# Optimization experiments

Measured on AMD Instinct MI355X. Metric: run time of the kernel, lower is better.

The kernel has to match this reference:

```python
import jax, jax.numpy as jnp
import numpy as np
from jax import lax

NPOINT = 1024
NSAMPLE = 32
RADIUS = 0.2
EPS = 1e-5  # BatchNorm eps (torch default)


def farthest_point_sample(xyz, npoint):
    # xyz: [B, N, 3] -> [B, npoint] int32 indices. Deterministic start at index 0
    # (torch version uses a random start; math is otherwise identical).
    B, N, _ = xyz.shape

    def step(carry, _):
        distance, farthest = carry
        centroid = jnp.take_along_axis(xyz, farthest[:, None, None], axis=1)  # [B,1,3]
        d = jnp.sum((xyz - centroid) ** 2, axis=-1)                            # [B,N]
        distance = jnp.minimum(distance, d)
        return (distance, jnp.argmax(distance, axis=-1).astype(jnp.int32)), farthest

    init = (jnp.full((B, N), 1e10, xyz.dtype), jnp.zeros((B,), jnp.int32))
    _, cents = lax.scan(step, init, None, length=npoint)  # [npoint, B]
    return cents.T


def query_ball_point(radius, nsample, xyz, new_xyz):
    # xyz: [B,N,3], new_xyz: [B,S,3] -> [B,S,nsample] int32 indices
    B, N, _ = xyz.shape
    S = new_xyz.shape[1]
    sqr = jnp.sum((new_xyz[:, :, None, :] - xyz[:, None, :, :]) ** 2, axis=-1)  # [B,S,N]
    base = jnp.broadcast_to(jnp.arange(N, dtype=jnp.int32), (B, S, N))
    idx = jnp.where(sqr > radius * radius, N, base)
    idx = jnp.sort(idx, axis=-1)[:, :, :nsample]
    first = idx[:, :, :1]
    return jnp.where(idx == N, first, idx)


def index_points(points, idx):
    # points: [B,N,C], idx: [B,...] -> [B,...,C]
    return jax.vmap(lambda p, i: p[i])(points, idx)


def conv_bn_relu(x, w, b, g, beta):
    # 1x1 Conv2d == per-point linear; BatchNorm2d in training mode (batch stats,
    # biased variance) over all dims except channel.
    y = jnp.einsum('bskc,oc->bsko', x, w) + b          # [B,S,K,O]
    m = jnp.mean(y, axis=(0, 1, 2), keepdims=True)
    v = jnp.var(y, axis=(0, 1, 2), keepdims=True)
    return jax.nn.relu((y - m) / jnp.sqrt(v + EPS) * g + beta)


def setup_inputs() -> dict:
    key = jax.random.key(0)
    ks = jax.random.split(key, 8)
    B, N, D = 16, 4096, 64
    xyz = jax.random.uniform(ks[0], (B, N, 3), dtype=jnp.float32)
    points = jax.random.normal(ks[1], (B, N, D), dtype=jnp.float32)
    chans = [D + 3, 64, 64, 128]
    inp = {'xyz': xyz, 'points': points}
    for i in range(3):
        cin, cout = chans[i], chans[i + 1]
        inp[f'w{i}'] = jax.random.normal(ks[2 + i], (cout, cin), dtype=jnp.float32) * (1.0 / np.sqrt(cin))
        inp[f'b{i}'] = jnp.zeros((cout,), jnp.float32)
        inp[f'g{i}'] = jnp.ones((cout,), jnp.float32)
        inp[f'be{i}'] = jnp.zeros((cout,), jnp.float32)
    return inp


def reference(xyz, points, w0, b0, g0, be0, w1, b1, g1, be1, w2, b2, g2, be2):
    fps_idx = farthest_point_sample(xyz, NPOINT)            # [B,S]
    new_xyz = index_points(xyz, fps_idx)                    # [B,S,3]
    group_idx = query_ball_point(RADIUS, NSAMPLE, xyz, new_xyz)  # [B,S,K]
    grouped_xyz = index_points(xyz, group_idx) - new_xyz[:, :, None, :]  # [B,S,K,3]
    feats = jnp.concatenate([grouped_xyz, index_points(points, group_idx)], axis=-1)
    for (w, b, g, be) in ((w0, b0, g0, be0), (w1, b1, g1, be1), (w2, b2, g2, be2)):
        feats = conv_bn_relu(feats, w, b, g, be)
    new_points = jnp.max(feats, axis=2)                     # max over nsample -> [B,S,C_out]
    return new_xyz, new_points
```

## Files before the change

kernel.cpp:

```cpp
#include <hip/hip_runtime.h>
#include <hip/hip_bf16.h>
#include <cstdint>
#include <cstddef>

#define NPTS   4096
#define NPT    1024
#define NSAMP  32
#define NBATCH 16
#define MROWS  (NBATCH*NPT*NSAMP)
#define EPSV   1e-5f

typedef __attribute__((ext_vector_type(8))) short bfrag;
typedef __attribute__((ext_vector_type(4))) float f32x4;

static __device__ __forceinline__ unsigned short f2bf(float f) {
  union { float f; unsigned u; } x; x.f = f;
  unsigned u = x.u;
  u += 0x7FFFu + ((u >> 16) & 1u);
  return (unsigned short)(u >> 16);
}
static __device__ __forceinline__ float bf2f(unsigned short h) {
  union { unsigned u; float f; } x; x.u = ((unsigned)h) << 16;
  return x.f;
}
static __device__ __forceinline__ unsigned cvt_pk_bf16(float lo, float hi) {
  unsigned r;
  asm("v_cvt_pk_bf16_f32 %0, %1, %2" : "=v"(r) : "v"(lo), "v"(hi));
  return r;
}

__global__ __launch_bounds__(256) void prep_kernel(
    const float* __restrict__ w0, const float* __restrict__ w1,
    const float* __restrict__ w2, unsigned short* __restrict__ wb0,
    unsigned short* __restrict__ wb1, unsigned short* __restrict__ wb2) {
  const int tid = threadIdx.x;
  for (int i = tid; i < 64 * 96; i += 256) {
    const int o = i / 96, c = i % 96;
    wb0[i] = (c < 67) ? f2bf(w0[o * 67 + c]) : (unsigned short)0;
  }
  for (int i = tid; i < 64 * 64; i += 256) wb1[i] = f2bf(w1[i]);
  for (int i = tid; i < 128 * 64; i += 256) wb2[i] = f2bf(w2[i]);
}

#define FPS_T 256
#define PPT   (NPTS / FPS_T)

template <int CTRL>
static __device__ __forceinline__ float dpp_max_step(float v) {
  int t = __builtin_amdgcn_update_dpp(0, __float_as_int(v), CTRL, 0xF, 0xF, true);
  return fmaxf(v, __int_as_float(t));
}

__global__ __launch_bounds__(FPS_T) void fps_kernel(
    const float* __restrict__ xyz, float* __restrict__ out_newxyz) {
  __shared__ __align__(16) float xs[NPTS];
  __shared__ __align__(16) float ys[NPTS];
  __shared__ __align__(16) float zs[NPTS];
  __shared__ float wv_[4];
  __shared__ int   wi_[4];

  const int b = blockIdx.x;
  const int tid = threadIdx.x;
  const int wave = tid >> 6;
  const float* base = xyz + (size_t)b * NPTS * 3;
  for (int i = tid; i < NPTS; i += FPS_T) {
    xs[i] = base[3 * i + 0];
    ys[i] = base[3 * i + 1];
    zs[i] = base[3 * i + 2];
  }
  __syncthreads();

  const int p0 = tid * PPT;
  float px[PPT], py[PPT], pz[PPT], dist[PPT];
  #pragma unroll
  for (int i = 0; i < PPT; i += 4) {
    *(float4*)&px[i] = *(const float4*)&xs[p0 + i];
    *(float4*)&py[i] = *(const float4*)&ys[p0 + i];
    *(float4*)&pz[i] = *(const float4*)&zs[p0 + i];
  }
  #pragma unroll
  for (int i = 0; i < PPT; ++i) dist[i] = 1e10f;

  int cur = 0;
  float* outb = out_newxyz + (size_t)b * NPT * 3;
  for (int it = 0; it < NPT; ++it) {
    const float cx = xs[cur], cy = ys[cur], cz = zs[cur];
    if (tid == 0) {
      outb[3 * it + 0] = cx;
      outb[3 * it + 1] = cy;
      outb[3 * it + 2] = cz;
    }
    if (it == NPT - 1) break;

    float bestv = -1.f; int besti = p0;
    #pragma unroll
    for (int i = 0; i < PPT; ++i) {
      const float dx = __fsub_rn(px[i], cx);
      const float dy = __fsub_rn(py[i], cy);
      const float dz = __fsub_rn(pz[i], cz);
      const float d = __fadd_rn(__fadd_rn(__fmul_rn(dx, dx), __fmul_rn(dy, dy)),
                                __fmul_rn(dz, dz));
      const float nd = fminf(dist[i], d);
      dist[i] = nd;
      const bool g = nd > bestv;
      bestv = g ? nd : bestv;
      besti = g ? (p0 + i) : besti;
    }

    float m = bestv;
    m = dpp_max_step<0x111>(m);
    m = dpp_max_step<0x112>(m);
    m = dpp_max_step<0x114>(m);
    m = dpp_max_step<0x118>(m);
    m = dpp_max_step<0x142>(m);
    m = dpp_max_step<0x143>(m);
    const float wmax =
        __int_as_float(__builtin_amdgcn_readlane(__float_as_int(m), 63));

    const unsigned long long mask = __ballot(bestv == wmax);
    const int wl = __ffsll((long long)mask) - 1;
    const int widx = __builtin_amdgcn_readlane(besti, wl);

    if ((tid & 63) == 0) { wv_[wave] = wmax; wi_[wave] = widx; }
    __syncthreads();
    float bv = wv_[0]; int bi = wi_[0];
    #pragma unroll
    for (int w = 1; w < 4; ++w) {
      const float v = wv_[w]; const int i2 = wi_[w];
      const bool g = v > bv;
      bv = g ? v : bv; bi = g ? i2 : bi;
    }
    cur = bi;
    __syncthreads();
  }
}

__global__ __launch_bounds__(256) void ballquery_kernel(
    const float* __restrict__ xyz, const float* __restrict__ newxyz,
    int* __restrict__ gidx) {
  const int gw = (int)((blockIdx.x * 256 + threadIdx.x) >> 6);
  const int lane = threadIdx.x & 63;
  const int b = gw >> 10, s = gw & 1023;
  const float* base = xyz + (size_t)b * NPTS * 3;
  const float* c = newxyz + (size_t)(b * NPT + s) * 3;
  const float cx = c[0], cy = c[1], cz = c[2];
  const float R2 = (float)(0.2 * 0.2);
  int* g = gidx + (size_t)(b * NPT + s) * NSAMP;

  int count = 0;
  int first = -1;
  for (int ch = 0; ch < NPTS / 64; ++ch) {
    const int i = ch * 64 + lane;
    const float dx = __fsub_rn(base[3 * i + 0], cx);
    const float dy = __fsub_rn(base[3 * i + 1], cy);
    const float dz = __fsub_rn(base[3 * i + 2], cz);
    const float d = __fadd_rn(__fadd_rn(__fmul_rn(dx, dx), __fmul_rn(dy, dy)),
                              __fmul_rn(dz, dz));
    const bool pred = !(d > R2);
    const unsigned long long mask = __ballot(pred);
    if (mask) {
      if (count == 0) first = ch * 64 + (__ffsll((long long)mask) - 1);
      const int rank = __popcll(mask & ((1ull << lane) - 1ull));
      const int pos = count + rank;
      if (pred && pos < NSAMP) g[pos] = i;
      count += (int)__popcll(mask);
      if (count >= NSAMP) break;
    }
  }
  if (first < 0) first = 0;
  for (int j = count + lane; j < NSAMP; j += 64) g[j] = first;
}

__global__ __launch_bounds__(256) void mm1_mfma_kernel(
    const float* __restrict__ xyz, const float* __restrict__ points,
    const float* __restrict__ newxyz, const int* __restrict__ gidx,
    const unsigned short* __restrict__ Wb, unsigned short* __restrict__ Y,
    float* __restrict__ psum, float* __restrict__ psq) {
  constexpr int KP = 104;
  __shared__ __align__(16) unsigned short As[64 * KP];
  __shared__ __align__(16) unsigned short ly[64 * 64];
  __shared__ float ssum[64], ssq[64];
  const int tid = threadIdx.x, bid = blockIdx.x;
  const size_t r0 = (size_t)bid * 64;

  {
    const int row = tid >> 2, q = tid & 3;
    const int gs = bid * 2 + (row >> 5);
    const int b = gs >> 10;
    const int k = row & 31;
    const int gpt = gidx[(size_t)gs * NSAMP + k];
    const float* px = xyz + ((size_t)b * NPTS + gpt) * 3;
    const float* pc = newxyz + (size_t)gs * 3;
    const float* pf = points + ((size_t)b * NPTS + gpt) * 64;
    float v[24];
    #pragma unroll
    for (int cc = 0; cc < 24; ++cc) {
      const int cch = q * 24 + cc;
      float val;
      if (cch < 3)       val = px[cch] - pc[cch];
      else if (cch < 67) val = pf[cch - 3];
      else               val = 0.f;
      v[cc] = val;
    }
    unsigned* dst = (unsigned*)&As[row * KP + q * 24];
    #pragma unroll
    for (int p = 0; p < 12; ++p) dst[p] = cvt_pk_bf16(v[2 * p], v[2 * p + 1]);
  }
  if (tid < 64) { ssum[tid] = 0.f; ssq[tid] = 0.f; }
  __syncthreads();

  const int wave = tid >> 6, lane = tid & 63;
  const int l15 = lane & 15, kq = lane >> 4;
  const unsigned short* abase = &As[(wave * 16 + l15) * KP + kq * 8];
  const bfrag a0 = *(const bfrag*)abase;
  const bfrag a1 = *(const bfrag*)(abase + 32);
  const bfrag a2 = *(const bfrag*)(abase + 64);

  #pragma unroll
  for (int nt = 0; nt < 4; ++nt) {
    const unsigned short* wsrc = Wb + (size_t)(nt * 16 + l15) * 96 + kq * 8;
    const bfrag b0 = *(const bfrag*)wsrc;
    const bfrag b1 = *(const bfrag*)(wsrc + 32);
    const bfrag b2 = *(const bfrag*)(wsrc + 64);
    f32x4 acc = {0.f, 0.f, 0.f, 0.f};
    acc = __builtin_amdgcn_mfma_f32_16x16x32_bf16(a0, b0, acc, 0, 0, 0);
    acc = __builtin_amdgcn_mfma_f32_16x16x32_bf16(a1, b1, acc, 0, 0, 0);
    acc = __builtin_amdgcn_mfma_f32_16x16x32_bf16(a2, b2, acc, 0, 0, 0);

    float s = acc[0] + acc[1] + acc[2] + acc[3];
    float q = acc[0]*acc[0] + acc[1]*acc[1] + acc[2]*acc[2] + acc[3]*acc[3];
    s += __shfl_xor(s, 16); q += __shfl_xor(q, 16);
    s += __shfl_xor(s, 32); q += __shfl_xor(q, 32);
    if (kq == 0) {
      atomicAdd(&ssum[nt * 16 + l15], s);
      atomicAdd(&ssq [nt * 16 + l15], q);
    }
    const unsigned p01 = cvt_pk_bf16(acc[0], acc[1]);
    const unsigned p23 = cvt_pk_bf16(acc[2], acc[3]);
    const int colo = nt * 16 + l15;
    const int rbase = wave * 16 + kq * 4;
    ly[(rbase + 0) * 64 + colo] = (unsigned short)(p01 & 0xffffu);
    ly[(rbase + 1) * 64 + colo] = (unsigned short)(p01 >> 16);
    ly[(rbase + 2) * 64 + colo] = (unsigned short)(p23 & 0xffffu);
    ly[(rbase + 3) * 64 + colo] = (unsigned short)(p23 >> 16);
  }
  __syncthreads();
  {
    const uint4* lsrc = (const uint4*)ly;
    uint4* gdst = (uint4*)(Y + r0 * 64);
    #pragma unroll
    for (int i = tid; i < 64 * 64 * 2 / 16; i += 256) gdst[i] = lsrc[i];
  }
  if (tid < 64) {
    psum[(size_t)bid * 64 + tid] = ssum[tid];
    psq [(size_t)bid * 64 + tid] = ssq [tid];
  }
}

static __device__ __forceinline__ bfrag affine_relu_frag(
    const unsigned short* __restrict__ src, const float* __restrict__ st,
    int c0) {
  union { bfrag f; unsigned u[4]; } r;
  const uint4 raw = *(const uint4*)src;
  const unsigned w[4] = {raw.x, raw.y, raw.z, raw.w};
  #pragma unroll
  for (int p = 0; p < 4; ++p) {
    const int c = c0 + 2 * p;
    float lo = bf2f((unsigned short)(w[p] & 0xffffu));
    float hi = bf2f((unsigned short)(w[p] >> 16));
    lo = fmaxf(fmaf(lo, st[2 * c + 0], st[2 * c + 1]), 0.f);
    hi = fmaxf(fmaf(hi, st[2 * c + 2], st[2 * c + 3]), 0.f);
    r.u[p] = cvt_pk_bf16(lo, hi);
  }
  return r.f;
}

template <int COUT, int WAVES>
__global__ __launch_bounds__(WAVES * 64) void mm_mfma_kernel(
    const unsigned short* __restrict__ Xin, const unsigned short* __restrict__ Wb,
    const float* __restrict__ stin, unsigned short* __restrict__ Y,
    float* __restrict__ psum, float* __restrict__ psq) {
  constexpr int NT = COUT / 16;
  constexpr int ROWS = WAVES * 16;
  __shared__ float ssum[COUT], ssq[COUT];
  __shared__ __align__(16) unsigned short ly[ROWS * COUT];
  const int tid = threadIdx.x, bid = blockIdx.x;
  const int wave = tid >> 6, lane = tid & 63;
  const int l15 = lane & 15, kq = lane >> 4;
  const size_t r0 = (size_t)bid * ROWS;
  if (tid < COUT) { ssum[tid] = 0.f; ssq[tid] = 0.f; }

  const int arow = wave * 16 + l15;
  const unsigned short* asrc = Xin + (r0 + arow) * 64 + kq * 8;
  const bfrag a0 = affine_relu_frag(asrc, stin, kq * 8);
  const bfrag a1 = affine_relu_frag(asrc + 32, stin, 32 + kq * 8);
  __syncthreads();

  #pragma unroll
  for (int nt = 0; nt < NT; ++nt) {
    const unsigned short* wsrc = Wb + (size_t)(nt * 16 + l15) * 64 + kq * 8;
    const bfrag b0 = *(const bfrag*)wsrc;
    const bfrag b1 = *(const bfrag*)(wsrc + 32);
    f32x4 acc = {0.f, 0.f, 0.f, 0.f};
    acc = __builtin_amdgcn_mfma_f32_16x16x32_bf16(a0, b0, acc, 0, 0, 0);
    acc = __builtin_amdgcn_mfma_f32_16x16x32_bf16(a1, b1, acc, 0, 0, 0);

    float s = acc[0] + acc[1] + acc[2] + acc[3];
    float q = acc[0]*acc[0] + acc[1]*acc[1] + acc[2]*acc[2] + acc[3]*acc[3];
    s += __shfl_xor(s, 16); q += __shfl_xor(q, 16);
    s += __shfl_xor(s, 32); q += __shfl_xor(q, 32);
    if (kq == 0) {
      atomicAdd(&ssum[nt * 16 + l15], s);
      atomicAdd(&ssq [nt * 16 + l15], q);
    }
    const unsigned p01 = cvt_pk_bf16(acc[0], acc[1]);
    const unsigned p23 = cvt_pk_bf16(acc[2], acc[3]);
    const int colo = nt * 16 + l15;
    const int rbase = wave * 16 + kq * 4;
    ly[(rbase + 0) * COUT + colo] = (unsigned short)(p01 & 0xffffu);
    ly[(rbase + 1) * COUT + colo] = (unsigned short)(p01 >> 16);
    ly[(rbase + 2) * COUT + colo] = (unsigned short)(p23 & 0xffffu);
    ly[(rbase + 3) * COUT + colo] = (unsigned short)(p23 >> 16);
  }
  __syncthreads();
  {
    const uint4* lsrc = (const uint4*)ly;
    uint4* gdst = (uint4*)(Y + r0 * COUT);
    #pragma unroll
    for (int i = tid; i < ROWS * COUT * 2 / 16; i += WAVES * 64) gdst[i] = lsrc[i];
  }
  if (tid < COUT) {
    psum[(size_t)bid * COUT + tid] = ssum[tid];
    psq [(size_t)bid * COUT + tid] = ssq [tid];
  }
}

__global__ __launch_bounds__(256) void finalize_kernel(
    const float* __restrict__ psum, const float* __restrict__ psq,
    const float* __restrict__ gam, const float* __restrict__ bet,
    float* __restrict__ st, int C, int nb) {
  const int c = blockIdx.x, tid = threadIdx.x;
  float s = 0.f, q = 0.f;
  for (int i = tid; i < nb; i += 256) {
    s += psum[(size_t)i * C + c];
    q += psq [(size_t)i * C + c];
  }
  #pragma unroll
  for (int off = 32; off > 0; off >>= 1) {
    s += __shfl_down(s, off);
    q += __shfl_down(q, off);
  }
  __shared__ float as_[4], aq_[4];
  if ((tid & 63) == 0) { as_[tid >> 6] = s; aq_[tid >> 6] = q; }
  __syncthreads();
  if (tid == 0) {
    s = as_[0] + as_[1] + as_[2] + as_[3];
    q = aq_[0] + aq_[1] + aq_[2] + aq_[3];
    const float invM = 1.f / (float)MROWS;
    const float mean = s * invM;
    const float var = q * invM - mean * mean;
    const float inv = 1.f / sqrtf(var + EPSV);
    const float sc = gam[c] * inv;
    st[2 * c + 0] = sc;
    st[2 * c + 1] = bet[c] - mean * sc;
  }
}

__global__ __launch_bounds__(128) void maxpool_kernel(
    const unsigned short* __restrict__ Y3, const float* __restrict__ st,
    float* __restrict__ out) {
  const int bsi = blockIdx.x, c = threadIdx.x;
  const unsigned short* p = Y3 + (size_t)bsi * NSAMP * 128 + c;
  const float sc = st[2 * c], sh = st[2 * c + 1];
  float m = -1e30f;
  #pragma unroll 8
  for (int k = 0; k < NSAMP; ++k)
    m = fmaxf(m, fmaf(bf2f(p[(size_t)k * 128]), sc, sh));
  out[(size_t)bsi * 128 + c] = fmaxf(m, 0.f);
}

extern "C" void kernel_launch(void* const* d_in, const int* in_sizes, int n_in,
                              void* d_out, int out_size, void* d_ws, size_t ws_size,
                              hipStream_t stream) {
  (void)in_sizes; (void)n_in; (void)out_size; (void)ws_size;
  const float* xyz    = (const float*)d_in[0];
  const float* points = (const float*)d_in[1];
  const float* w0 = (const float*)d_in[2];
  const float* g0 = (const float*)d_in[4];
  const float* be0 = (const float*)d_in[5];
  const float* w1 = (const float*)d_in[6];
  const float* g1 = (const float*)d_in[8];
  const float* be1 = (const float*)d_in[9];
  const float* w2 = (const float*)d_in[10];
  const float* g2 = (const float*)d_in[12];
  const float* be2 = (const float*)d_in[13];

  float* out = (float*)d_out;
  float* newxyz = out;
  float* newpts = out + (size_t)NBATCH * NPT * 3;

  char* ws = (char*)d_ws;
  unsigned short* Y1 = (unsigned short*)ws;
  unsigned short* Y3 = (unsigned short*)ws;
  unsigned short* Y2 = (unsigned short*)(ws + 134217728);
  int*   gidx = (int*)  (ws + 201326592);
  float* psum = (float*)(ws + 203423744);
  float* psq  = (float*)(ws + 205520896);
  float* st   = (float*)(ws + 207618048);
  float* st1 = st, *st2 = st + 256, *st3 = st + 512;
  unsigned short* wb0 = (unsigned short*)(ws + 207621120);
  unsigned short* wb1 = (unsigned short*)(ws + 207621120 + 12288);
  unsigned short* wb2 = (unsigned short*)(ws + 207621120 + 12288 + 8192);

  prep_kernel<<<1, 256, 0, stream>>>(w0, w1, w2, wb0, wb1, wb2);
  fps_kernel<<<NBATCH, FPS_T, 0, stream>>>(xyz, newxyz);
  ballquery_kernel<<<(NBATCH * NPT) / 4, 256, 0, stream>>>(xyz, newxyz, gidx);
  mm1_mfma_kernel<<<MROWS / 64, 256, 0, stream>>>(xyz, points, newxyz, gidx, wb0, Y1, psum, psq);
  finalize_kernel<<<64, 256, 0, stream>>>(psum, psq, g0, be0, st1, 64, MROWS / 64);
  mm_mfma_kernel<64, 4><<<MROWS / 64, 256, 0, stream>>>(Y1, wb1, st1, Y2, psum, psq);
  finalize_kernel<<<64, 256, 0, stream>>>(psum, psq, g1, be1, st2, 64, MROWS / 64);
  mm_mfma_kernel<128, 8><<<MROWS / 128, 512, 0, stream>>>(Y2, wb2, st2, Y3, psum, psq);
  finalize_kernel<<<128, 256, 0, stream>>>(psum, psq, g2, be2, st3, 128, MROWS / 128);
  maxpool_kernel<<<NBATCH * NPT, 128, 0, stream>>>(Y3, st3, newpts);
}
```

Before: 951.5 us.

## Double-buffer FPS reduction slots, widen block to 512 threads, stage output in LDS

The farthest-point-sampling kernel now runs 512 threads per batch, so each thread holds 8 points instead of 16. Per-wave partial maxima go into a double-buffered shared array, which lets one barrier per iteration replace two. They are read back as vector loads and reduced across 8 waves. Sampled centroids are collected in shared memory and written to global with coalesced float4 stores at the end, instead of one thread writing scalars each iteration. The trade-off is a longer cross-wave reduction and more waves meeting at each barrier, in return for less per-thread serial work on a kernel that launches only 16 blocks.

```diff
diff --git a/kernel.cpp b/kernel.cpp
--- a/kernel.cpp
+++ b/kernel.cpp
@@ -42,7 +42,7 @@
   for (int i = tid; i < 128 * 64; i += 256) wb2[i] = f2bf(w2[i]);
 }
 
-#define FPS_T 256
+#define FPS_T 512
 #define PPT   (NPTS / FPS_T)
 
 template <int CTRL>
@@ -56,8 +56,8 @@
   __shared__ __align__(16) float xs[NPTS];
   __shared__ __align__(16) float ys[NPTS];
   __shared__ __align__(16) float zs[NPTS];
-  __shared__ float wv_[4];
-  __shared__ int   wi_[4];
+  __shared__ __align__(16) float olds[NPT * 3];
+  __shared__ __align__(16) uint2 sl[2][8];
 
   const int b = blockIdx.x;
   const int tid = threadIdx.x;
@@ -82,13 +82,12 @@
   for (int i = 0; i < PPT; ++i) dist[i] = 1e10f;
 
   int cur = 0;
-  float* outb = out_newxyz + (size_t)b * NPT * 3;
   for (int it = 0; it < NPT; ++it) {
     const float cx = xs[cur], cy = ys[cur], cz = zs[cur];
     if (tid == 0) {
-      outb[3 * it + 0] = cx;
-      outb[3 * it + 1] = cy;
-      outb[3 * it + 2] = cz;
+      olds[3 * it + 0] = cx;
+      olds[3 * it + 1] = cy;
+      olds[3 * it + 2] = cz;
     }
     if (it == NPT - 1) break;
 
@@ -121,18 +120,38 @@
     const int wl = __ffsll((long long)mask) - 1;
     const int widx = __builtin_amdgcn_readlane(besti, wl);
 
-    if ((tid & 63) == 0) { wv_[wave] = wmax; wi_[wave] = widx; }
+    const int buf = it & 1;
+    if ((tid & 63) == 0)
+      sl[buf][wave] = make_uint2(__float_as_uint(wmax), (unsigned)widx);
     __syncthreads();
-    float bv = wv_[0]; int bi = wi_[0];
-    #pragma unroll
-    for (int w = 1; w < 4; ++w) {
-      const float v = wv_[w]; const int i2 = wi_[w];
-      const bool g = v > bv;
-      bv = g ? v : bv; bi = g ? i2 : bi;
+
+    const uint4* p4 = (const uint4*)&sl[buf][0];
+    const uint4 q0 = p4[0], q1 = p4[1], q2 = p4[2], q3 = p4[3];
+    float bv; int bi;
+    {
+      bv = __uint_as_float(q0.x); bi = (int)q0.y;
+      const float v1 = __uint_as_float(q0.z);
+      if (v1 > bv) { bv = v1; bi = (int)q0.w; }
+      const float v2 = __uint_as_float(q1.x);
+      if (v2 > bv) { bv = v2; bi = (int)q1.y; }
+      const float v3 = __uint_as_float(q1.z);
+      if (v3 > bv) { bv = v3; bi = (int)q1.w; }
+      const float v4 = __uint_as_float(q2.x);
+      if (v4 > bv) { bv = v4; bi = (int)q2.y; }
+      const float v5 = __uint_as_float(q2.z);
+      if (v5 > bv) { bv = v5; bi = (int)q2.w; }
+      const float v6 = __uint_as_float(q3.x);
+      if (v6 > bv) { bv = v6; bi = (int)q3.y; }
+      const float v7 = __uint_as_float(q3.z);
+      if (v7 > bv) { bv = v7; bi = (int)q3.w; }
     }
     cur = bi;
-    __syncthreads();
-  }
+  }
+
+  __syncthreads();
+  float* outb = out_newxyz + (size_t)b * NPT * 3;
+  for (int i = tid; i < NPT * 3 / 4; i += FPS_T)
+    *(float4*)&outb[4 * i] = *(const float4*)&olds[4 * i];
 }
 
 __global__ __launch_bounds__(256) void ballquery_kernel(
```

Result: slower. 1.011 ms (+6.3%).

## Restructure FPS loop with packed math, coordinate carry, and single barrier

Applied to the files above, without the earlier changes.

The farthest-point-sampling kernel now keeps each thread's points in registers as packed float2 pairs and computes distances with v_pk_add/v_pk_mul. It carries the winning point's coordinates through the reduction instead of an index, so no shared-memory lookup of the centroid is needed. A double-buffered shared slot removes the second barrier per iteration. Outputs are staged in LDS and written with vectorized stores at the end. Risks: the packed ops change the rounding of (p-c)^2 from the separate sub/mul/add sequence, and ties now resolve by in-thread tree order rather than first index, so selected points may differ from the reference.

```diff
diff --git a/kernel.cpp b/kernel.cpp
--- a/kernel.cpp
+++ b/kernel.cpp
@@ -12,6 +12,7 @@
 
 typedef __attribute__((ext_vector_type(8))) short bfrag;
 typedef __attribute__((ext_vector_type(4))) float f32x4;
+typedef __attribute__((ext_vector_type(2))) float f32x2;
 
 static __device__ __forceinline__ unsigned short f2bf(float f) {
   union { float f; unsigned u; } x; x.f = f;
@@ -27,6 +28,16 @@
   unsigned r;
   asm("v_cvt_pk_bf16_f32 %0, %1, %2" : "=v"(r) : "v"(lo), "v"(hi));
   return r;
+}
+static __device__ __forceinline__ f32x2 pk_add(f32x2 a, f32x2 b) {
+  f32x2 d;
+  asm("v_pk_add_f32 %0, %1, %2" : "=v"(d) : "v"(a), "v"(b));
+  return d;
+}
+static __device__ __forceinline__ f32x2 pk_mul(f32x2 a, f32x2 b) {
+  f32x2 d;
+  asm("v_pk_mul_f32 %0, %1, %2" : "=v"(d) : "v"(a), "v"(b));
+  return d;
 }
 
 __global__ __launch_bounds__(256) void prep_kernel(
@@ -53,61 +64,79 @@
 
 __global__ __launch_bounds__(FPS_T) void fps_kernel(
     const float* __restrict__ xyz, float* __restrict__ out_newxyz) {
-  __shared__ __align__(16) float xs[NPTS];
-  __shared__ __align__(16) float ys[NPTS];
-  __shared__ __align__(16) float zs[NPTS];
-  __shared__ float wv_[4];
-  __shared__ int   wi_[4];
+  __shared__ __align__(16) float olds[NPT * 3];
+  __shared__ __align__(16) float4 sl[2][4];
 
   const int b = blockIdx.x;
   const int tid = threadIdx.x;
   const int wave = tid >> 6;
   const float* base = xyz + (size_t)b * NPTS * 3;
-  for (int i = tid; i < NPTS; i += FPS_T) {
-    xs[i] = base[3 * i + 0];
-    ys[i] = base[3 * i + 1];
-    zs[i] = base[3 * i + 2];
-  }
-  __syncthreads();
-
-  const int p0 = tid * PPT;
-  float px[PPT], py[PPT], pz[PPT], dist[PPT];
+
+  float arr[48];
+  {
+    const float* src = base + tid * 48;
+    #pragma unroll
+    for (int i = 0; i < 12; ++i)
+      *(float4*)&arr[4 * i] = *(const float4*)&src[4 * i];
+  }
+  f32x2 px2[8], py2[8], pz2[8], dist2[8];
   #pragma unroll
-  for (int i = 0; i < PPT; i += 4) {
-    *(float4*)&px[i] = *(const float4*)&xs[p0 + i];
-    *(float4*)&py[i] = *(const float4*)&ys[p0 + i];
-    *(float4*)&pz[i] = *(const float4*)&zs[p0 + i];
-  }
-  #pragma unroll
-  for (int i = 0; i < PPT; ++i) dist[i] = 1e10f;
-
-  int cur = 0;
-  float* outb = out_newxyz + (size_t)b * NPT * 3;
+  for (int p = 0; p < 8; ++p) {
+    px2[p] = f32x2{arr[6 * p + 0], arr[6 * p + 3]};
+    py2[p] = f32x2{arr[6 * p + 1], arr[6 * p + 4]};
+    pz2[p] = f32x2{arr[6 * p + 2], arr[6 * p + 5]};
+    dist2[p] = f32x2{1e10f, 1e10f};
+  }
+
+  float ccx = base[0], ccy = base[1], ccz = base[2];
+
   for (int it = 0; it < NPT; ++it) {
-    const float cx = xs[cur], cy = ys[cur], cz = zs[cur];
     if (tid == 0) {
-      outb[3 * it + 0] = cx;
-      outb[3 * it + 1] = cy;
-      outb[3 * it + 2] = cz;
+      olds[3 * it + 0] = ccx;
+      olds[3 * it + 1] = ccy;
+      olds[3 * it + 2] = ccz;
     }
     if (it == NPT - 1) break;
 
-    float bestv = -1.f; int besti = p0;
-    #pragma unroll
-    for (int i = 0; i < PPT; ++i) {
-      const float dx = __fsub_rn(px[i], cx);
-      const float dy = __fsub_rn(py[i], cy);
-      const float dz = __fsub_rn(pz[i], cz);
-      const float d = __fadd_rn(__fadd_rn(__fmul_rn(dx, dx), __fmul_rn(dy, dy)),
-                                __fmul_rn(dz, dz));
-      const float nd = fminf(dist[i], d);
-      dist[i] = nd;
-      const bool g = nd > bestv;
-      bestv = g ? nd : bestv;
-      besti = g ? (p0 + i) : besti;
-    }
-
-    float m = bestv;
+    const f32x2 ncx = {-ccx, -ccx}, ncy = {-ccy, -ccy}, ncz = {-ccz, -ccz};
+    #pragma unroll
+    for (int p = 0; p < 8; ++p) {
+      const f32x2 dx = pk_add(px2[p], ncx);
+      const f32x2 dy = pk_add(py2[p], ncy);
+      const f32x2 dz = pk_add(pz2[p], ncz);
+      const f32x2 t1 = pk_mul(dx, dx);
+      const f32x2 t2 = pk_mul(dy, dy);
+      const f32x2 t3 = pk_mul(dz, dz);
+      const f32x2 s = pk_add(pk_add(t1, t2), t3);
+      f32x2 nd = dist2[p];
+      nd.x = fminf(nd.x, s.x);
+      nd.y = fminf(nd.y, s.y);
+      dist2[p] = nd;
+    }
+
+    float tv[8], tx[8], ty[8], tz[8];
+    #pragma unroll
+    for (int p = 0; p < 8; ++p) {
+      const f32x2 d2 = dist2[p];
+      const bool g = d2.y > d2.x;
+      tv[p] = g ? d2.y : d2.x;
+      tx[p] = g ? px2[p].y : px2[p].x;
+      ty[p] = g ? py2[p].y : py2[p].x;
+      tz[p] = g ? pz2[p].y : pz2[p].x;
+    }
+    #pragma unroll
+    for (int st = 4; st >= 1; st >>= 1) {
+      #pragma unroll
+      for (int p = 0; p < st; ++p) {
+        const bool g = tv[p + st] > tv[p];
+        tv[p] = g ? tv[p + st] : tv[p];
+        tx[p] = g ? tx[p + st] : tx[p];
+        ty[p] = g ? ty[p + st] : ty[p];
+        tz[p] = g ? tz[p + st] : tz[p];
+      }
+    }
+
+    float m = tv[0];
     m = dpp_max_step<0x111>(m);
     m = dpp_max_step<0x112>(m);
     m = dpp_max_step<0x114>(m);
@@ -117,22 +146,32 @@
     const float wmax =
         __int_as_float(__builtin_amdgcn_readlane(__float_as_int(m), 63));
 
-    const unsigned long long mask = __ballot(bestv == wmax);
+    const unsigned long long mask = __ballot(tv[0] == wmax);
     const int wl = __ffsll((long long)mask) - 1;
-    const int widx = __builtin_amdgcn_readlane(besti, wl);
-
-    if ((tid & 63) == 0) { wv_[wave] = wmax; wi_[wave] = widx; }
+    const float bx =
+        __int_as_float(__builtin_amdgcn_readlane(__float_as_int(tx[0]), wl));
+    const float by =
+        __int_as_float(__builtin_amdgcn_readlane(__float_as_int(ty[0]), wl));
+    const float bz =
+        __int_as_float(__builtin_amdgcn_readlane(__float_as_int(tz[0]), wl));
+
+    const int buf = it & 1;
+    if ((tid & 63) == 0) sl[buf][wave] = make_float4(wmax, bx, by, bz);
     __syncthreads();
-    float bv = wv_[0]; int bi = wi_[0];
-    #pragma unroll
-    for (int w = 1; w < 4; ++w) {
-      const float v = wv_[w]; const int i2 = wi_[w];
-      const bool g = v > bv;
-      bv = g ? v : bv; bi = g ? i2 : bi;
-    }
-    cur = bi;
-    __syncthreads();
-  }
+
+    const float4 s0 = sl[buf][0], s1 = sl[buf][1];
+    const float4 s2 = sl[buf][2], s3 = sl[buf][3];
+    float bv = s0.x;
+    ccx = s0.y; ccy = s0.z; ccz = s0.w;
+    if (s1.x > bv) { bv = s1.x; ccx = s1.y; ccy = s1.z; ccz = s1.w; }
+    if (s2.x > bv) { bv = s2.x; ccx = s2.y; ccy = s2.z; ccz = s2.w; }
+    if (s3.x > bv) { bv = s3.x; ccx = s3.y; ccy = s3.z; ccz = s3.w; }
+  }
+
+  __syncthreads();
+  float* outb = out_newxyz + (size_t)b * NPT * 3;
+  for (int i = tid; i < NPT * 3 / 4; i += FPS_T)
+    *(float4*)&outb[4 * i] = *(const float4*)&olds[4 * i];
 }
 
 __global__ __launch_bounds__(256) void ballquery_kernel(
```

After: 1.441 ms. 1.51x slower.
